# Optimization experiments

Measured on AMD Instinct MI355X. Metric: run time of the kernel, lower is better.

The kernel has to match this reference:

```python
import jax, jax.numpy as jnp
import numpy as np

N_NODES = 100000
N_EDGES = 1600000
N_GRAPHS = 64
F = 50
N_LAYERS = 3
EPS_STD = 1e-5
EPS_BN = 1e-5


def _glorot(key, shape):
    fan_in, fan_out = shape[0], shape[1]
    lim = float(np.sqrt(6.0 / (fan_in + fan_out)))
    return jax.random.uniform(key, shape, jnp.float32, -lim, lim)


def setup_inputs() -> dict:
    key = jax.random.key(0)
    ks = jax.random.split(key, 20)
    x = jax.random.normal(ks[0], (N_NODES, 2), jnp.float32)
    edge_index = jax.random.randint(ks[1], (2, N_EDGES), 0, N_NODES, jnp.int32)
    batch_ids = jnp.sort(jax.random.randint(ks[2], (N_NODES,), 0, N_GRAPHS, jnp.int32))
    inp = {
        "x": x,
        "edge_index": edge_index,
        "batch_ids": batch_ids,
        "W_gcn": _glorot(ks[3], (2, F)),
        "b_gcn": jnp.zeros((F,), jnp.float32),
        # stacked per-layer PNA params [L, ...]
        "pre_W": jnp.stack([_glorot(jax.random.fold_in(ks[4], i), (2 * F, F)) for i in range(N_LAYERS)]),
        "pre_b": jnp.zeros((N_LAYERS, F), jnp.float32),
        "post_W": jnp.stack([_glorot(jax.random.fold_in(ks[5], i), (13 * F, F)) for i in range(N_LAYERS)]),
        "post_b": jnp.zeros((N_LAYERS, F), jnp.float32),
        "lin_W": jnp.stack([_glorot(jax.random.fold_in(ks[6], i), (F, F)) for i in range(N_LAYERS)]),
        "lin_b": jnp.zeros((N_LAYERS, F), jnp.float32),
        "bn_gamma": jnp.ones((N_LAYERS, F), jnp.float32),
        "bn_beta": jnp.zeros((N_LAYERS, F), jnp.float32),
        "mlp_W1": _glorot(ks[7], (F, 25)),
        "mlp_b1": jnp.zeros((25,), jnp.float32),
        "mlp_W2": _glorot(ks[8], (25, 1)),
        "mlp_b2": jnp.zeros((1,), jnp.float32),
    }
    return inp


def _pna_layer(x, src, dst, deg_raw, deg_c, avg_log, Wp, bp, Wq, bq, Wl, bl):
    # pre-NN on messages: concat(x_i, x_j) -> F   (i = target/dst, j = source/src)
    h = jnp.concatenate([x[dst], x[src]], axis=-1) @ Wp + bp  # [E, F]
    dc = deg_c[:, None]
    s = jax.ops.segment_sum(h, dst, num_segments=N_NODES)
    mean = s / dc
    mean_sq = jax.ops.segment_sum(h * h, dst, num_segments=N_NODES) / dc
    var = jax.nn.relu(mean_sq - mean * mean)
    std = jnp.sqrt(var + EPS_STD)
    has_edge = (deg_raw > 0)[:, None]
    mn = jnp.where(has_edge, jax.ops.segment_min(h, dst, num_segments=N_NODES), 0.0)
    mx = jnp.where(has_edge, jax.ops.segment_max(h, dst, num_segments=N_NODES), 0.0)
    agg = jnp.concatenate([mean, mn, mx, std], axis=-1)  # [N, 4F]
    amp = (jnp.log1p(deg_c) / avg_log)[:, None]
    att = (avg_log / jnp.log1p(deg_c))[:, None]
    out = jnp.concatenate([agg, agg * amp, agg * att], axis=-1)  # [N, 12F]
    out = jnp.concatenate([x, out], axis=-1) @ Wq + bq  # post-NN: [N, 13F] -> F
    return out @ Wl + bl


def reference(x, edge_index, batch_ids, W_gcn, b_gcn, pre_W, pre_b, post_W, post_b,
              lin_W, lin_b, bn_gamma, bn_beta, mlp_W1, mlp_b1, mlp_W2, mlp_b2):
    src, dst = edge_index[0], edge_index[1]

    # ---- GCNConv(2 -> 50) with self loops + symmetric normalization ----
    h = x @ W_gcn
    loop = jnp.arange(N_NODES, dtype=src.dtype)
    src_a = jnp.concatenate([src, loop])
    dst_a = jnp.concatenate([dst, loop])
    deg_sl = jax.ops.segment_sum(jnp.ones_like(src_a, jnp.float32), dst_a, num_segments=N_NODES)
    dinv = jnp.where(deg_sl > 0, jax.lax.rsqrt(deg_sl), 0.0)
    norm = (dinv[src_a] * dinv[dst_a])[:, None]
    h = jax.ops.segment_sum(h[src_a] * norm, dst_a, num_segments=N_NODES) + b_gcn

    # ---- degree stats for PNA scalers ----
    deg_raw = jax.ops.segment_sum(jnp.ones_like(src, jnp.float32), dst, num_segments=N_NODES)
    deg_c = jnp.maximum(deg_raw, 1.0)
    avg_log = jnp.mean(jnp.log1p(deg_raw))

    for l in range(N_LAYERS):
        h = _pna_layer(h, src, dst, deg_raw, deg_c, avg_log,
                       pre_W[l], pre_b[l], post_W[l], post_b[l], lin_W[l], lin_b[l])
        mu = jnp.mean(h, axis=0)
        var = jnp.mean((h - mu) ** 2, axis=0)
        h = (h - mu) * jax.lax.rsqrt(var + EPS_BN) * bn_gamma[l] + bn_beta[l]
        h = jax.nn.relu(h)

    # ---- global add pool + MLP (dropout is identity at eval) ----
    g = jax.ops.segment_sum(h, batch_ids, num_segments=N_GRAPHS)  # [G, F]
    g = jax.nn.relu(g @ mlp_W1 + mlp_b1)
    g = g @ mlp_W2 + mlp_b2  # [G, 1]
    return g.reshape(N_GRAPHS)
```

## Files before the change

### kernel.cpp

```cpp
#include <hip/hip_runtime.h>
#include <math.h>

#define NN 100000
#define NE 1600000
#define NG 64
#define FF 50
#define NL 3
#define NBUCK ((NN + 255) / 256)

typedef short bf16x8 __attribute__((ext_vector_type(8)));
typedef float f32x4 __attribute__((ext_vector_type(4)));

__device__ __forceinline__ short f2bf(float f) {
  return __builtin_bit_cast(short, (__bf16)f);
}
__device__ __forceinline__ float bf2f(short s) {
  unsigned int u = ((unsigned int)(unsigned short)s) << 16;
  return __builtin_bit_cast(float, u);
}
__device__ __forceinline__ float2 unpk2(unsigned u) {
  float2 v;
  v.x = __builtin_bit_cast(float, u << 16);
  v.y = __builtin_bit_cast(float, u & 0xFFFF0000u);
  return v;
}
__device__ __forceinline__ unsigned pk2(float2 v) {
  return (unsigned)(unsigned short)f2bf(v.x) | ((unsigned)(unsigned short)f2bf(v.y) << 16);
}

__device__ __forceinline__ bf16x8 ldfrag_bn(const short* base, const float2* __restrict__ ab, int kbase) {
  bf16x8 raw = *(const bf16x8*)base;
  unsigned u[4];
  __builtin_memcpy(u, &raw, 16);
  short t[8] __attribute__((aligned(16)));
#pragma unroll
  for (int i = 0; i < 4; ++i) {
    float2 v = unpk2(u[i]);
    float2 a0 = ab[kbase + 2 * i], a1 = ab[kbase + 2 * i + 1];
    v.x = fmaxf(fmaf(v.x, a0.x, a0.y), 0.f);
    v.y = fmaxf(fmaf(v.y, a1.x, a1.y), 0.f);
    ((unsigned*)t)[i] = pk2(v);
  }
  bf16x8 r;
  __builtin_memcpy(&r, t, 16);
  return r;
}

__global__ void k_deg(const int* __restrict__ dst, int* __restrict__ deg) {
  int e = blockIdx.x * blockDim.x + threadIdx.x;
  if (e < NE) atomicAdd(&deg[dst[e]], 1);
}

__global__ void k_scan1(const int* __restrict__ deg, int* __restrict__ off, int* __restrict__ parts) {
  __shared__ int sm[1024];
  int i = blockIdx.x * 1024 + threadIdx.x;
  int v = (i < NN) ? deg[i] : 0;
  sm[threadIdx.x] = v;
  __syncthreads();
  for (int ofs = 1; ofs < 1024; ofs <<= 1) {
    int t = (threadIdx.x >= ofs) ? sm[threadIdx.x - ofs] : 0;
    __syncthreads();
    sm[threadIdx.x] += t;
    __syncthreads();
  }
  if (i < NN) off[i] = sm[threadIdx.x] - v;
  if (threadIdx.x == 1023) parts[blockIdx.x] = sm[1023];
}

__global__ void k_scan2(int* __restrict__ parts, int nb) {
  __shared__ int sm[128];
  int v = (threadIdx.x < nb) ? parts[threadIdx.x] : 0;
  sm[threadIdx.x] = v;
  __syncthreads();
  for (int ofs = 1; ofs < 128; ofs <<= 1) {
    int t = (threadIdx.x >= ofs) ? sm[threadIdx.x - ofs] : 0;
    __syncthreads();
    sm[threadIdx.x] += t;
    __syncthreads();
  }
  if (threadIdx.x < nb) parts[threadIdx.x] = sm[threadIdx.x] - v;
}

__global__ void k_scan3(int* __restrict__ off, const int* __restrict__ parts, int* __restrict__ bcur) {
  int i = blockIdx.x * 256 + threadIdx.x;
  if (i < NN) {
    int v = off[i] + parts[i >> 10];
    off[i] = v;
    if ((i & 255) == 0) bcur[i >> 8] = v;
  }
  if (i == 0) off[NN] = NE;
}

__global__ void k_nodeinit(const int* __restrict__ deg, float* __restrict__ dinv,
                           float* __restrict__ lgc, float* __restrict__ scal) {
  int i = blockIdx.x * 256 + threadIdx.x;
  float lp = 0.f;
  if (i < NN) {
    int d = deg[i];
    dinv[i] = rsqrtf((float)(d + 1));
    int dc = d > 1 ? d : 1;
    lgc[i] = log1pf((float)dc);
    lp = log1pf((float)d);
  }
  for (int o = 32; o > 0; o >>= 1) lp += __shfl_down(lp, o);
  __shared__ float red[4];
  int lane = threadIdx.x & 63, w = threadIdx.x >> 6;
  if (lane == 0) red[w] = lp;
  __syncthreads();
  if (threadIdx.x == 0) atomicAdd(scal, red[0] + red[1] + red[2] + red[3]);
}

__global__ __launch_bounds__(256) void k_bucket(const int* __restrict__ src, const int* __restrict__ dst,
                                                int* __restrict__ bcur, unsigned* __restrict__ tmp) {
  __shared__ int hist[NBUCK];
  __shared__ int base[NBUCK];
  int t = threadIdx.x;
  for (int i = t; i < NBUCK; i += 256) hist[i] = 0;
  __syncthreads();
  int e0 = blockIdx.x * 4096;
  int myb[16], myrank[16];
  unsigned mypack[16];
#pragma unroll
  for (int i = 0; i < 16; ++i) {
    int e = e0 + i * 256 + t;
    if (e < NE) {
      int s = src[e], d = dst[e];
      int b = d >> 8;
      myb[i] = b;
      mypack[i] = ((unsigned)(d & 255) << 17) | (unsigned)s;
      myrank[i] = atomicAdd(&hist[b], 1);
    } else myb[i] = -1;
  }
  __syncthreads();
  for (int i = t; i < NBUCK; i += 256)
    base[i] = hist[i] ? atomicAdd(&bcur[i], hist[i]) : 0;
  __syncthreads();
#pragma unroll
  for (int i = 0; i < 16; ++i)
    if (myb[i] >= 0) tmp[base[myb[i]] + myrank[i]] = mypack[i];
}

__global__ __launch_bounds__(256) void k_bsort(const int* __restrict__ off, const unsigned* __restrict__ tmp,
                                               int* __restrict__ ssrc) {
  int b = blockIdx.x;
  int n0 = b * 256;
  int nEnd = n0 + 256 < NN ? n0 + 256 : NN;
  __shared__ int cnt[256];
  __shared__ int nb[256];
  int t = threadIdx.x;
  cnt[t] = 0;
  if (n0 + t < nEnd) nb[t] = off[n0 + t];
  __syncthreads();
  int lo = off[n0], hiE = off[nEnd];
  for (int e = lo + t; e < hiE; e += 256) {
    unsigned p = tmp[e];
    int dloc = p >> 17;
    int s = (int)(p & 0x1FFFFu);
    int pos = nb[dloc] + atomicAdd(&cnt[dloc], 1);
    ssrc[pos] = s;
  }
}

__global__ void k_fusew(const float* __restrict__ postW, const float* __restrict__ postb,
                        const float* __restrict__ linW, const float* __restrict__ linb,
                        float* __restrict__ A, float* __restrict__ bias2) {
  int wid = (blockIdx.x * blockDim.x + threadIdx.x) >> 6;
  int f = threadIdx.x & 63;
  if (wid >= 3 * 651) return;
  int l = wid / 651, r = wid % 651;
  int fc = f < FF ? f : FF - 1;
  const float* lw = linW + l * FF * FF;
  float acc = 0.f;
  if (r < 650) {
    const float* pw = postW + (l * 650 + r) * FF;
    for (int j = 0; j < FF; ++j) acc += pw[j] * lw[j * FF + fc];
    if (f < FF) A[(l * 650 + r) * FF + f] = acc;
  } else {
    const float* pb = postb + l * FF;
    for (int j = 0; j < FF; ++j) acc += pb[j] * lw[j * FF + fc];
    bias2[l * 64 + f] = (f < FF) ? (acc + linb[l * FF + f]) : 0.f;
  }
}

__global__ void k_packA(const float* __restrict__ Af, short* __restrict__ Abt) {
  int t = blockIdx.x * 256 + threadIdx.x;
  if (t >= 3 * 13 * 64 * 64) return;
  int kk = t & 63;
  int f = (t >> 6) & 63;
  int lc = t >> 12;
  int c = lc % 13;
  int l = lc / 13;
  float v = 0.f;
  if (kk < FF && f < FF) v = Af[((size_t)(l * 650 + c * FF + kk)) * FF + f];
  Abt[t] = f2bf(v);
}

__global__ void k_packP(const float* __restrict__ preW, short* __restrict__ Pbt) {
  int t = blockIdx.x * 256 + threadIdx.x;
  if (t >= NL * 2 * 64 * 64) return;
  int kk = t & 63;
  int f = (t >> 6) & 63;
  int ls = t >> 12;
  int s = ls & 1, l = ls >> 1;
  float v = 0.f;
  if (kk < FF && f < FF) v = preW[(size_t)(l * 100 + s * FF + kk) * FF + f];
  Pbt[t] = f2bf(v);
}

__global__ void k_gcnpre(const float* __restrict__ x, const float* __restrict__ Wg,
                         const float* __restrict__ dinv, short* __restrict__ pb) {
  int t = blockIdx.x * 256 + threadIdx.x;
  int n = t >> 6, f = t & 63;
  if (n >= NN) return;
  float v = 0.f;
  if (f < FF) v = (x[2 * n] * Wg[f] + x[2 * n + 1] * Wg[FF + f]) * dinv[n];
  pb[n * 64 + f] = f2bf(v);
}

__global__ void k_gcnagg(const short* __restrict__ pb, const int* __restrict__ off,
                         const int* __restrict__ ssrc, const float* __restrict__ dinv,
                         const float* __restrict__ bg, short* __restrict__ hb) {
  int wid = (blockIdx.x * blockDim.x + threadIdx.x) >> 6;
  int lane = threadIdx.x & 63;
  if (wid >= NN) return;
  int n = wid;
  int p = lane & 31;
  int hf = lane >> 5;
  float2 acc;
  {
    float2 sv = unpk2(*(const unsigned*)(pb + n * 64 + 2 * p));
    acc.x = hf ? 0.f : sv.x;
    acc.y = hf ? 0.f : sv.y;
  }
  int lo = off[n], hi = off[n + 1];
  for (int base = lo; base < hi; base += 64) {
    int rem = hi - base;
    int cnt = rem > 64 ? 64 : rem;
    int sidx = (base + lane < hi) ? ssrc[base + lane] : 0;
    int pairs = cnt >> 1;
    int j = 0;
    for (; j + 4 <= pairs; j += 4) {
#pragma unroll
      for (int i = 0; i < 4; ++i) {
        int s = __shfl(sidx, 2 * (j + i) + hf);
        float2 v = unpk2(*(const unsigned*)(pb + s * 64 + 2 * p));
        acc.x += v.x; acc.y += v.y;
      }
    }
    for (; j < pairs; ++j) {
      int s = __shfl(sidx, 2 * j + hf);
      float2 v = unpk2(*(const unsigned*)(pb + s * 64 + 2 * p));
      acc.x += v.x; acc.y += v.y;
    }
    if (cnt & 1) {
      int s = __shfl(sidx, cnt - 1);
      float2 v = unpk2(*(const unsigned*)(pb + s * 64 + 2 * p));
      if (hf == 0) { acc.x += v.x; acc.y += v.y; }
    }
  }
  acc.x += __shfl_xor(acc.x, 32);
  acc.y += __shfl_xor(acc.y, 32);
  if (lane < 32) {
    float2 o = make_float2(0.f, 0.f);
    if (p < 25) {
      float dv = dinv[n];
      float2 bgp = *(const float2*)(bg + 2 * p);
      o = make_float2(dv * acc.x + bgp.x, dv * acc.y + bgp.y);
    }
    ((unsigned*)(hb + n * 64))[p] = pk2(o);
  }
}

__global__ __launch_bounds__(256) void k_preM(const short* __restrict__ hin, const float2* __restrict__ ab,
                                              const short* __restrict__ Pbt, const float* __restrict__ preb,
                                              short* __restrict__ cbh, short* __restrict__ bbh, int l) {
  int tid = threadIdx.x;
  int w = tid >> 6, lane = tid & 63;
  int q = lane >> 4, m16 = lane & 15;
  int n0 = blockIdx.x * 64 + w * 16;
  int anode = n0 + m16;
  int nsafe = anode < NN ? anode : 0;
  bf16x8 afr[2];
#pragma unroll
  for (int hh = 0; hh < 2; ++hh) {
    const short* srcp = hin + (size_t)nsafe * 64 + hh * 32 + q * 8;
    afr[hh] = ab ? ldfrag_bn(srcp, ab, hh * 32 + q * 8) : *(const bf16x8*)srcp;
  }
  const short* P0 = Pbt + l * 8192;
  f32x4 aT[4], aB2[4];
#pragma unroll
  for (int ft = 0; ft < 4; ++ft) {
    aT[ft] = (f32x4){0.f, 0.f, 0.f, 0.f};
    aB2[ft] = (f32x4){0.f, 0.f, 0.f, 0.f};
  }
#pragma unroll
  for (int hh = 0; hh < 2; ++hh) {
#pragma unroll
    for (int ft = 0; ft < 4; ++ft) {
      bf16x8 b0 = *(const bf16x8*)(P0 + ((ft * 16 + m16) << 6) + hh * 32 + q * 8);
      bf16x8 b1 = *(const bf16x8*)(P0 + 4096 + ((ft * 16 + m16) << 6) + hh * 32 + q * 8);
      aT[ft] = __builtin_amdgcn_mfma_f32_16x16x32_bf16(afr[hh], b0, aT[ft], 0, 0, 0);
      aB2[ft] = __builtin_amdgcn_mfma_f32_16x16x32_bf16(afr[hh], b1, aB2[ft], 0, 0, 0);
    }
  }
#pragma unroll
  for (int r = 0; r < 4; ++r) {
    int node = n0 + q * 4 + r;
    if (node >= NN) continue;
#pragma unroll
    for (int ft = 0; ft < 4; ++ft) {
      int col = ft * 16 + m16;
      cbh[node * 64 + col] = (col < FF) ? f2bf(aT[ft][r] + preb[l * FF + col]) : 0;
      bbh[node * 64 + col] = f2bf(aB2[ft][r]);
    }
  }
}

__global__ void k_agg(const short* __restrict__ bbh, const short* __restrict__ cbh,
                      const int* __restrict__ off, const int* __restrict__ ssrc,
                      const float* __restrict__ lgc, const float* __restrict__ scal,
                      short* __restrict__ agb, float* __restrict__ ampatt) {
  int wid = (blockIdx.x * blockDim.x + threadIdx.x) >> 6;
  int lane = threadIdx.x & 63;
  if (wid >= NN) return;
  int n = wid;
  int p = lane & 31;
  int hf = lane >> 5;
  float2 S = {0.f, 0.f}, S2 = {0.f, 0.f};
  float2 MN = {INFINITY, INFINITY}, MX = {-INFINITY, -INFINITY};
  int lo = off[n], hi = off[n + 1];
  for (int base = lo; base < hi; base += 64) {
    int rem = hi - base;
    int cnt = rem > 64 ? 64 : rem;
    int sidx = (base + lane < hi) ? ssrc[base + lane] : 0;
    int pairs = cnt >> 1;
    int j = 0;
    for (; j + 4 <= pairs; j += 4) {
#pragma unroll
      for (int i = 0; i < 4; ++i) {
        int s = __shfl(sidx, 2 * (j + i) + hf);
        float2 v = unpk2(*(const unsigned*)(bbh + s * 64 + 2 * p));
        S.x += v.x; S.y += v.y;
        S2.x = fmaf(v.x, v.x, S2.x); S2.y = fmaf(v.y, v.y, S2.y);
        MN.x = fminf(MN.x, v.x); MN.y = fminf(MN.y, v.y);
        MX.x = fmaxf(MX.x, v.x); MX.y = fmaxf(MX.y, v.y);
      }
    }
    for (; j < pairs; ++j) {
      int s = __shfl(sidx, 2 * j + hf);
      float2 v = unpk2(*(const unsigned*)(bbh + s * 64 + 2 * p));
      S.x += v.x; S.y += v.y;
      S2.x = fmaf(v.x, v.x, S2.x); S2.y = fmaf(v.y, v.y, S2.y);
      MN.x = fminf(MN.x, v.x); MN.y = fminf(MN.y, v.y);
      MX.x = fmaxf(MX.x, v.x); MX.y = fmaxf(MX.y, v.y);
    }
    if (cnt & 1) {
      int s = __shfl(sidx, cnt - 1);
      float2 v = unpk2(*(const unsigned*)(bbh + s * 64 + 2 * p));
      if (hf == 0) {
        S.x += v.x; S.y += v.y;
        S2.x = fmaf(v.x, v.x, S2.x); S2.y = fmaf(v.y, v.y, S2.y);
        MN.x = fminf(MN.x, v.x); MN.y = fminf(MN.y, v.y);
        MX.x = fmaxf(MX.x, v.x); MX.y = fmaxf(MX.y, v.y);
      }
    }
  }
  S.x += __shfl_xor(S.x, 32);   S.y += __shfl_xor(S.y, 32);
  S2.x += __shfl_xor(S2.x, 32); S2.y += __shfl_xor(S2.y, 32);
  MN.x = fminf(MN.x, __shfl_xor(MN.x, 32)); MN.y = fminf(MN.y, __shfl_xor(MN.y, 32));
  MX.x = fmaxf(MX.x, __shfl_xor(MX.x, 32)); MX.y = fmaxf(MX.y, __shfl_xor(MX.y, 32));
  int d = hi - lo;
  bool valid = p < 25;
  float2 mean, mnv, mxv, stdv;
  if (d > 0) {
    float inv = 1.f / (float)d;
    float2 m = make_float2(S.x * inv, S.y * inv);
    float vx = S2.x * inv - m.x * m.x; vx = vx > 0.f ? vx : 0.f;
    float vy = S2.y * inv - m.y * m.y; vy = vy > 0.f ? vy : 0.f;
    stdv = make_float2(sqrtf(vx + 1e-5f), sqrtf(vy + 1e-5f));
    float2 c = valid ? unpk2(((const unsigned*)(cbh + n * 64))[p]) : make_float2(0.f, 0.f);
    mean = make_float2(c.x + m.x, c.y + m.y);
    mnv = make_float2(c.x + MN.x, c.y + MN.y);
    mxv = make_float2(c.x + MX.x, c.y + MX.y);
  } else {
    mean = mnv = mxv = make_float2(0.f, 0.f);
    float sq = sqrtf(1e-5f);
    stdv = make_float2(sq, sq);
  }
  if (lane < 32) {
    unsigned* row32 = (unsigned*)(agb + (size_t)n * 256);
    row32[p]      = valid ? pk2(mean) : 0u;
    row32[32 + p] = valid ? pk2(mnv) : 0u;
    row32[64 + p] = valid ? pk2(mxv) : 0u;
    row32[96 + p] = valid ? pk2(stdv) : 0u;
  }
  if (lane == 0) {
    float avg = scal[0] * (1.f / NN);
    float lg = lgc[n];
    ampatt[2 * n] = lg / avg;
    ampatt[2 * n + 1] = avg / lg;
  }
}

__global__ __launch_bounds__(256, 3) void k_gemm(const short* __restrict__ h, const float2* __restrict__ ab,
                                                 const short* __restrict__ agb, const float* __restrict__ ampatt,
                                                 const short* __restrict__ Abt, const float* __restrict__ bias2,
                                                 short* __restrict__ hout, float* __restrict__ bnsumR) {
  __shared__ short Bs[3][64][72];
  int tid = threadIdx.x;
  int w = tid >> 6, lane = tid & 63;
  int q = lane >> 4, m16 = lane & 15;
  int n0 = blockIdx.x * 64 + w * 16;

  int anode = n0 + m16;
  int nsafe = anode < NN ? anode : 0;
  bf16x8 afr[5][2];
  {
#pragma unroll
    for (int hh = 0; hh < 2; ++hh) {
      const short* srcp = h + (size_t)nsafe * 64 + hh * 32 + q * 8;
      afr[0][hh] = ab ? ldfrag_bn(srcp, ab, hh * 32 + q * 8) : *(const bf16x8*)srcp;
    }
    const short* arow = agb + (size_t)nsafe * 256;
#pragma unroll
    for (int c = 1; c <= 4; ++c)
#pragma unroll
      for (int hh = 0; hh < 2; ++hh)
        afr[c][hh] = *(const bf16x8*)(arow + (c - 1) * 64 + hh * 32 + q * 8);
  }

  f32x4 acc[3][4];
#pragma unroll
  for (int s = 0; s < 3; ++s)
#pragma unroll
    for (int ft = 0; ft < 4; ++ft) acc[s][ft] = (f32x4){0.f, 0.f, 0.f, 0.f};

  int bf = tid >> 2;
  int bko = (tid & 3) * 16;
  float4 rg[3][2];
  {
    const float4* g = (const float4*)(Abt + (bf << 6) + bko);
    rg[0][0] = g[0]; rg[0][1] = g[1];
  }
  for (int ph = 0; ph < 5; ++ph) {
    int nslice = (ph == 0) ? 1 : 3;
    if (ph) __syncthreads();
    for (int s = 0; s < nslice; ++s) {
      *(float4*)&Bs[s][bf][bko] = rg[s][0];
      *(float4*)&Bs[s][bf][bko + 8] = rg[s][1];
    }
    __syncthreads();
    if (ph < 4) {
#pragma unroll
      for (int s = 0; s < 3; ++s) {
        int chunk = (ph + 1) + 4 * s;
        const float4* g = (const float4*)(Abt + (chunk << 12) + (bf << 6) + bko);
        rg[s][0] = g[0]; rg[s][1] = g[1];
      }
    }
    if (ph == 0) {
#pragma unroll
      for (int hh = 0; hh < 2; ++hh)
#pragma unroll
        for (int ft = 0; ft < 4; ++ft) {
          bf16x8 b = *(const bf16x8*)&Bs[0][ft * 16 + m16][hh * 32 + q * 8];
          acc[0][ft] = __builtin_amdgcn_mfma_f32_16x16x32_bf16(afr[0][hh], b, acc[0][ft], 0, 0, 0);
        }
    } else {
#pragma unroll
      for (int hh = 0; hh < 2; ++hh)
#pragma unroll
        for (int s = 0; s < 3; ++s)
#pragma unroll
          for (int ft = 0; ft < 4; ++ft) {
            bf16x8 b = *(const bf16x8*)&Bs[s][ft * 16 + m16][hh * 32 + q * 8];
            acc[s][ft] = __builtin_amdgcn_mfma_f32_16x16x32_bf16(afr[ph][hh], b, acc[s][ft], 0, 0, 0);
          }
    }
  }

  float sacc[4] = {0.f, 0.f, 0.f, 0.f};
  float qacc[4] = {0.f, 0.f, 0.f, 0.f};
#pragma unroll
  for (int r = 0; r < 4; ++r) {
    int node = n0 + q * 4 + r;
    if (node >= NN) continue;
    float2 aa = *(const float2*)(ampatt + 2 * node);
#pragma unroll
    for (int ft = 0; ft < 4; ++ft) {
      int col = ft * 16 + m16;
      float val = 0.f;
      if (col < FF) {
        val = acc[0][ft][r] + aa.x * acc[1][ft][r] + aa.y * acc[2][ft][r] + bias2[col];
        sacc[ft] += val;
        qacc[ft] = fmaf(val, val, qacc[ft]);
      }
      hout[node * 64 + col] = f2bf(val);
    }
  }
#pragma unroll
  for (int ft = 0; ft < 4; ++ft) {
    sacc[ft] += __shfl_xor(sacc[ft], 16);
    sacc[ft] += __shfl_xor(sacc[ft], 32);
    qacc[ft] += __shfl_xor(qacc[ft], 16);
    qacc[ft] += __shfl_xor(qacc[ft], 32);
  }
  if (lane < 16) {
    float* bl = bnsumR + (blockIdx.x & 7) * 128;
#pragma unroll
    for (int ft = 0; ft < 4; ++ft) {
      int col = ft * 16 + lane;
      if (col < FF) {
        atomicAdd(&bl[col], sacc[ft]);
        atomicAdd(&bl[64 + col], qacc[ft]);
      }
    }
  }
}

__global__ void k_bnab(const float* __restrict__ bnsumR, const float* __restrict__ gamma,
                       const float* __restrict__ beta, float2* __restrict__ ab, int l) {
  int f = threadIdx.x;
  float a = 0.f, b = 0.f;
  if (f < FF) {
    float s = 0.f, q = 0.f;
    for (int r = 0; r < 8; ++r) { s += bnsumR[r * 128 + f]; q += bnsumR[r * 128 + 64 + f]; }
    float mu = s * (1.f / NN);
    float vq = q * (1.f / NN) - mu * mu;
    float rs = rsqrtf((vq > 0.f ? vq : 0.f) + 1e-5f);
    a = rs * gamma[l * FF + f];
    b = beta[l * FF + f] - mu * a;
  }
  ab[f] = make_float2(a, b);
}

__global__ void k_gsum(const short* __restrict__ h, const float2* __restrict__ ab,
                       const int* __restrict__ batch, float* __restrict__ gsum) {
  int w = threadIdx.x >> 6, lane = threadIdx.x & 63;
  int fc = lane < FF ? lane : FF - 1;
  bool act = lane < FF;
  float2 p = ab[fc];
  int n0 = blockIdx.x * 256 + w * 64;
  if (n0 >= NN) return;
  int nEnd = n0 + 64 < NN ? n0 + 64 : NN;
  float acc = 0.f;
  int gcur = batch[n0];
  for (int n = n0; n < nEnd; ++n) {
    int g = batch[n];
    if (g != gcur) {
      if (act) atomicAdd(&gsum[gcur * 64 + lane], acc);
      acc = 0.f; gcur = g;
    }
    float v = bf2f(h[n * 64 + fc]);
    acc += fmaxf(fmaf(v, p.x, p.y), 0.f);
  }
  if (act) atomicAdd(&gsum[gcur * 64 + lane], acc);
}

__global__ void k_mlp(const float* __restrict__ gsum, const float* __restrict__ W1,
                      const float* __restrict__ b1, const float* __restrict__ W2,
                      const float* __restrict__ b2, float* __restrict__ out) {
  int g = threadIdx.x;
  if (g >= NG) return;
  float gv[FF];
#pragma unroll
  for (int f = 0; f < FF; ++f) gv[f] = gsum[g * 64 + f];
  float r = b2[0];
  for (int j = 0; j < 25; ++j) {
    float a = b1[j];
#pragma unroll
    for (int f = 0; f < FF; ++f) a = fmaf(gv[f], W1[f * 25 + j], a);
    r += fmaxf(a, 0.f) * W2[j];
  }
  out[g] = r;
}

extern "C" void kernel_launch(void* const* d_in, const int* in_sizes, int n_in,
                              void* d_out, int out_size, void* d_ws, size_t ws_size,
                              hipStream_t stream) {
  const float* x     = (const float*)d_in[0];
  const int*   ei    = (const int*)d_in[1];
  const int*   src   = ei;
  const int*   dst   = ei + NE;
  const int*   batch = (const int*)d_in[2];
  const float* Wg    = (const float*)d_in[3];
  const float* bg    = (const float*)d_in[4];
  const float* preW  = (const float*)d_in[5];
  const float* preb  = (const float*)d_in[6];
  const float* postW = (const float*)d_in[7];
  const float* postb = (const float*)d_in[8];
  const float* linW  = (const float*)d_in[9];
  const float* linb  = (const float*)d_in[10];
  const float* gamma = (const float*)d_in[11];
  const float* beta  = (const float*)d_in[12];
  const float* W1    = (const float*)d_in[13];
  const float* b1    = (const float*)d_in[14];
  const float* W2    = (const float*)d_in[15];
  const float* b2    = (const float*)d_in[16];
  float* out = (float*)d_out;

  char* W = (char*)d_ws;
  int*    deg    = (int*)(W + 0);
  int*    off    = (int*)(W + 400384);
  int*    bcur   = (int*)(W + 801280);
  int*    parts  = (int*)(W + 803328);
  float*  dinv   = (float*)(W + 807424);
  float*  lgc    = (float*)(W + 1207808);
  float*  scal   = (float*)(W + 1608192);
  float*  bnsum  = (float*)(W + 1608704);
  float2* ab     = (float2*)(W + 1620992);
  float*  Af     = (float*)(W + 1622528);
  float*  bias2  = (float*)(W + 2012672);
  short*  Abt    = (short*)(W + 2013696);
  short*  Pbt    = (short*)(W + 2333184);
  unsigned* tmp  = (unsigned*)(W + 2382336);
  int*    ssrc   = (int*)(W + 8782336);
  short*  hA     = (short*)(W + 15182336);
  short*  hB     = (short*)(W + 27982592);
  short*  cbh    = (short*)(W + 40782848);
  short*  bbh    = (short*)(W + 53583104);
  short*  agb    = (short*)(W + 66383360);
  float*  ampatt = (float*)(W + 117583616);
  float*  gsum   = (float*)(W + 118383872);

  hipMemsetAsync(deg, 0, 400384, stream);
  hipMemsetAsync(scal, 0, 12800, stream);
  hipMemsetAsync(gsum, 0, 16384, stream);

  k_deg<<<(NE + 255) / 256, 256, 0, stream>>>(dst, deg);
  k_scan1<<<98, 1024, 0, stream>>>(deg, off, parts);
  k_scan2<<<1, 128, 0, stream>>>(parts, 98);
  k_scan3<<<(NN + 255) / 256, 256, 0, stream>>>(off, parts, bcur);
  k_nodeinit<<<(NN + 255) / 256, 256, 0, stream>>>(deg, dinv, lgc, scal);
  k_bucket<<<(NE + 4095) / 4096, 256, 0, stream>>>(src, dst, bcur, tmp);
  k_bsort<<<NBUCK, 256, 0, stream>>>(off, tmp, ssrc);
  k_fusew<<<(3 * 651 + 3) / 4, 256, 0, stream>>>(postW, postb, linW, linb, Af, bias2);
  k_packA<<<(3 * 13 * 64 * 64 + 255) / 256, 256, 0, stream>>>(Af, Abt);
  k_packP<<<(NL * 2 * 64 * 64 + 255) / 256, 256, 0, stream>>>(preW, Pbt);

  k_gcnpre<<<NN / 4, 256, 0, stream>>>(x, Wg, dinv, bbh);
  k_gcnagg<<<NN / 4, 256, 0, stream>>>(bbh, off, ssrc, dinv, bg, hA);

  short* hin = hA;
  short* hout = hB;
  for (int l = 0; l < NL; ++l) {
    const float2* abl = (l == 0) ? nullptr : (ab + (l - 1) * 64);
    k_preM<<<(NN + 63) / 64, 256, 0, stream>>>(hin, abl, Pbt, preb, cbh, bbh, l);
    k_agg<<<NN / 4, 256, 0, stream>>>(bbh, cbh, off, ssrc, lgc, scal, agb, ampatt);
    k_gemm<<<(NN + 63) / 64, 256, 0, stream>>>(hin, abl, agb, ampatt,
                                               Abt + l * 13 * 4096, bias2 + l * 64, hout,
                                               bnsum + l * 1024);
    k_bnab<<<1, 64, 0, stream>>>(bnsum + l * 1024, gamma, beta, ab + l * 64, l);
    short* t = hin; hin = hout; hout = t;
  }
  k_gsum<<<NBUCK, 256, 0, stream>>>(hin, ab + 2 * 64, batch, gsum);
  k_mlp<<<1, 64, 0, stream>>>(gsum, W1, b1, W2, b2, out);
}
```

Before: 783.8 us.

## Permute weight columns for vectorized 8-byte output stores, unroll gathers, raise occupancy

Weight packing now permutes output columns so each lane's four MFMA tiles map to four consecutive feature columns. Epilogues in the pre-GEMM and post-GEMM kernels can then write one 8-byte store per row instead of four scattered 2-byte stores, and bias loads are hoisted into registers. The aggregation kernels gain an 8-way unrolled gather loop to keep more loads in flight. k_gemm launch bounds are raised from 3 to 4 blocks per CU, which may force register spilling.

```diff
diff --git a/kernel.cpp b/kernel.cpp
--- a/kernel.cpp
+++ b/kernel.cpp
@@ -187,11 +187,12 @@
   if (t >= 3 * 13 * 64 * 64) return;
   int kk = t & 63;
   int f = (t >> 6) & 63;
+  int oc = 4 * (f & 15) + (f >> 4);
   int lc = t >> 12;
   int c = lc % 13;
   int l = lc / 13;
   float v = 0.f;
-  if (kk < FF && f < FF) v = Af[((size_t)(l * 650 + c * FF + kk)) * FF + f];
+  if (kk < FF && oc < FF) v = Af[((size_t)(l * 650 + c * FF + kk)) * FF + oc];
   Abt[t] = f2bf(v);
 }
 
@@ -200,10 +201,11 @@
   if (t >= NL * 2 * 64 * 64) return;
   int kk = t & 63;
   int f = (t >> 6) & 63;
+  int oc = 4 * (f & 15) + (f >> 4);
   int ls = t >> 12;
   int s = ls & 1, l = ls >> 1;
   float v = 0.f;
-  if (kk < FF && f < FF) v = preW[(size_t)(l * 100 + s * FF + kk) * FF + f];
+  if (kk < FF && oc < FF) v = preW[(size_t)(l * 100 + s * FF + kk) * FF + oc];
   Pbt[t] = f2bf(v);
 }
 
@@ -239,6 +241,14 @@
     int sidx = (base + lane < hi) ? ssrc[base + lane] : 0;
     int pairs = cnt >> 1;
     int j = 0;
+    for (; j + 8 <= pairs; j += 8) {
+#pragma unroll
+      for (int i = 0; i < 8; ++i) {
+        int s = __shfl(sidx, 2 * (j + i) + hf);
+        float2 v = unpk2(*(const unsigned*)(pb + s * 64 + 2 * p));
+        acc.x += v.x; acc.y += v.y;
+      }
+    }
     for (; j + 4 <= pairs; j += 4) {
 #pragma unroll
       for (int i = 0; i < 4; ++i) {
@@ -303,16 +313,26 @@
       aB2[ft] = __builtin_amdgcn_mfma_f32_16x16x32_bf16(afr[hh], b1, aB2[ft], 0, 0, 0);
     }
   }
+  float pb4[4];
+#pragma unroll
+  for (int ft = 0; ft < 4; ++ft) {
+    int col = 4 * m16 + ft;
+    pb4[ft] = (col < FF) ? preb[l * FF + col] : 0.f;
+  }
 #pragma unroll
   for (int r = 0; r < 4; ++r) {
     int node = n0 + q * 4 + r;
     if (node >= NN) continue;
+    short cs[4] __attribute__((aligned(8)));
+    short bs[4] __attribute__((aligned(8)));
 #pragma unroll
     for (int ft = 0; ft < 4; ++ft) {
-      int col = ft * 16 + m16;
-      cbh[node * 64 + col] = (col < FF) ? f2bf(aT[ft][r] + preb[l * FF + col]) : 0;
-      bbh[node * 64 + col] = f2bf(aB2[ft][r]);
-    }
+      int col = 4 * m16 + ft;
+      cs[ft] = (col < FF) ? f2bf(aT[ft][r] + pb4[ft]) : (short)0;
+      bs[ft] = f2bf(aB2[ft][r]);
+    }
+    *(uint2*)(cbh + node * 64 + 4 * m16) = *(const uint2*)cs;
+    *(uint2*)(bbh + node * 64 + 4 * m16) = *(const uint2*)bs;
   }
 }
 
@@ -335,6 +355,17 @@
     int sidx = (base + lane < hi) ? ssrc[base + lane] : 0;
     int pairs = cnt >> 1;
     int j = 0;
+    for (; j + 8 <= pairs; j += 8) {
+#pragma unroll
+      for (int i = 0; i < 8; ++i) {
+        int s = __shfl(sidx, 2 * (j + i) + hf);
+        float2 v = unpk2(*(const unsigned*)(bbh + s * 64 + 2 * p));
+        S.x += v.x; S.y += v.y;
+        S2.x = fmaf(v.x, v.x, S2.x); S2.y = fmaf(v.y, v.y, S2.y);
+        MN.x = fminf(MN.x, v.x); MN.y = fminf(MN.y, v.y);
+        MX.x = fmaxf(MX.x, v.x); MX.y = fmaxf(MX.y, v.y);
+      }
+    }
     for (; j + 4 <= pairs; j += 4) {
 #pragma unroll
       for (int i = 0; i < 4; ++i) {
@@ -402,7 +433,7 @@
   }
 }
 
-__global__ __launch_bounds__(256, 3) void k_gemm(const short* __restrict__ h, const float2* __restrict__ ab,
+__global__ __launch_bounds__(256, 4) void k_gemm(const short* __restrict__ h, const float2* __restrict__ ab,
                                                  const short* __restrict__ agb, const float* __restrict__ ampatt,
                                                  const short* __restrict__ Abt, const float* __restrict__ bias2,
                                                  short* __restrict__ hout, float* __restrict__ bnsumR) {
@@ -479,6 +510,9 @@
     }
   }
 
+  float b4[4];
+#pragma unroll
+  for (int ft = 0; ft < 4; ++ft) b4[ft] = bias2[4 * m16 + ft];
   float sacc[4] = {0.f, 0.f, 0.f, 0.f};
   float qacc[4] = {0.f, 0.f, 0.f, 0.f};
 #pragma unroll
@@ -486,17 +520,15 @@
     int node = n0 + q * 4 + r;
     if (node >= NN) continue;
     float2 aa = *(const float2*)(ampatt + 2 * node);
+    short st[4] __attribute__((aligned(8)));
 #pragma unroll
     for (int ft = 0; ft < 4; ++ft) {
-      int col = ft * 16 + m16;
-      float val = 0.f;
-      if (col < FF) {
-        val = acc[0][ft][r] + aa.x * acc[1][ft][r] + aa.y * acc[2][ft][r] + bias2[col];
-        sacc[ft] += val;
-        qacc[ft] = fmaf(val, val, qacc[ft]);
-      }
-      hout[node * 64 + col] = f2bf(val);
-    }
+      float val = acc[0][ft][r] + aa.x * acc[1][ft][r] + aa.y * acc[2][ft][r] + b4[ft];
+      st[ft] = f2bf(val);
+      sacc[ft] += val;
+      qacc[ft] = fmaf(val, val, qacc[ft]);
+    }
+    *(uint2*)(hout + node * 64 + 4 * m16) = *(const uint2*)st;
   }
 #pragma unroll
   for (int ft = 0; ft < 4; ++ft) {
@@ -509,7 +541,7 @@
     float* bl = bnsumR + (blockIdx.x & 7) * 128;
 #pragma unroll
     for (int ft = 0; ft < 4; ++ft) {
-      int col = ft * 16 + lane;
+      int col = 4 * lane + ft;
       if (col < FF) {
         atomicAdd(&bl[col], sacc[ft]);
         atomicAdd(&bl[64 + col], qacc[ft]);
```

After: 866.4 us. 10.5% more time.
